# Performance work log

Measured on AMD Instinct MI355X. Metric: run time of the kernel, lower is better.

## Reference

```python
import jax, jax.numpy as jnp
import numpy as np

N_LEAVES = 4096
NF = N_LEAVES            # one-hot leaf feature dim
NN = 2 * N_LEAVES - 1    # nodes in binary backbone tree
HID = 512
T_MIN, T_MAX = 0.0, 1.0  # time_grid endpoints


def _belief_prop(node_sample, ch0, ch1, parent):
    """Postorder c/d recursion then preorder correction, as in node_embedding_site_backbone.
    Node ids are topologically ordered (children < parent), so postorder = 0..NN-1."""
    is_leaf = node_sample >= 0
    leaf_d = jax.nn.one_hot(jnp.clip(node_sample, 0), NF, dtype=jnp.float32)
    c0 = jnp.zeros((NN,), jnp.float32)
    d0 = jnp.zeros((NN, NF), jnp.float32)

    def post(carry, u):
        c, d = carry
        cc = c[ch0[u]] + c[ch1[u]]
        dd = d[ch0[u]] + d[ch1[u]]
        cu = 1.0 / (3.0 - cc)
        du = cu * dd
        cu = jnp.where(is_leaf[u], 0.0, cu)
        du = jnp.where(is_leaf[u], leaf_d[u], du)
        return (c.at[u].set(cu), d.at[u].set(du)), None

    (c, d), _ = jax.lax.scan(post, (c0, d0), jnp.arange(NN))
    root = NN - 1

    def pre(d, u):
        du = jnp.where(u == root, d[u], c[u] * d[parent[u]] + d[u])
        return d.at[u].set(du), None

    d, _ = jax.lax.scan(pre, d, jnp.arange(NN - 1, -1, -1))
    return d


def _gcn_layer(x, neigh, W, b):
    # neighbor-list GCN: mean over {self} U valid neighbors, then linear
    n = x.shape[0]
    safe = jnp.where(neigh < 0, n, neigh)  # -1 -> extra zero row
    x_ext = jnp.concatenate([x, jnp.zeros((1, x.shape[1]), x.dtype)], axis=0)
    deg = 1.0 + jnp.sum(neigh >= 0, axis=1).astype(x.dtype)
    agg = (x + x_ext[safe].sum(axis=1)) / deg[:, None]
    return agg @ W + b


def setup_inputs():
    rng = np.random.default_rng(0)
    ch0 = -np.ones(NN, np.int64)
    ch1 = -np.ones(NN, np.int64)
    parent = -np.ones(NN, np.int64)
    avail = list(range(N_LEAVES))
    for u in range(N_LEAVES, NN):  # random binary coalescent topology
        a = avail.pop(int(rng.integers(len(avail))))
        b = avail.pop(int(rng.integers(len(avail))))
        ch0[u], ch1[u] = a, b
        parent[a] = u
        parent[b] = u
        avail.append(u)
    root = NN - 1
    node_sample = np.where(np.arange(NN) < N_LEAVES, np.arange(NN), -1).astype(np.int64)
    neigh = -np.ones((NN + 1, 3), np.int64)
    for u in range(NN):
        if u == root:
            neigh[u] = [ch0[u], ch1[u], -1]
        else:
            neigh[u] = [parent[u], ch0[u], ch1[u]]
    branch_child = np.arange(NN, dtype=np.int64)
    is_root = (branch_child == root).astype(np.float32)

    key = jax.random.key(0)
    ks = jax.random.split(key, 8)
    w = lambda k, s: jax.random.normal(k, s, jnp.float32) * 0.02
    E = 4 * HID + 2
    return {
        "node_sample": jnp.asarray(node_sample),
        "ch0": jnp.asarray(ch0),
        "ch1": jnp.asarray(ch1),
        "parent": jnp.asarray(parent),
        "neigh": jnp.asarray(neigh),
        "branch_child": jnp.asarray(branch_child),
        "current_focal_leaf": 7,
        "time_value": jax.random.uniform(ks[0], (NN,), jnp.float32),
        "is_root": jnp.asarray(is_root),
        "W_gnn1": w(ks[1], (NF, HID)), "b_gnn1": jnp.zeros((HID,), jnp.float32),
        "W_gnn2": w(ks[2], (HID, HID)), "b_gnn2": jnp.zeros((HID,), jnp.float32),
        "W_h1": w(ks[3], (E, HID)), "b_h1": jnp.zeros((HID,), jnp.float32),
        "W_h2": w(ks[4], (HID, HID)), "b_h2": jnp.zeros((HID,), jnp.float32),
        "W_h3": w(ks[5], (HID, 1)), "b_h3": jnp.zeros((1,), jnp.float32),
    }


def reference(node_sample, ch0, ch1, parent, neigh, branch_child, current_focal_leaf,
              time_value, is_root, W_gnn1, b_gnn1, W_gnn2, b_gnn2,
              W_h1, b_h1, W_h2, b_h2, W_h3, b_h3):
    d = _belief_prop(node_sample, ch0, ch1, parent)                  # (NN, NF)
    focal_feat = jax.nn.one_hot(current_focal_leaf, NF, dtype=jnp.float32)
    x = jnp.concatenate([d, focal_feat[None, :]], axis=0)            # (NN+1, NF)

    h = jax.nn.relu(_gcn_layer(x, neigh, W_gnn1, b_gnn1))
    emb = _gcn_layer(h, neigh, W_gnn2, b_gnn2)                       # (NN+1, HID)

    h_focal = emb[NN]                                                # appended focal node
    h_tgt = emb[branch_child]                                        # (A, HID)
    h_f = jnp.broadcast_to(h_focal[None, :], h_tgt.shape)
    t_norm = (time_value - T_MIN) / (T_MAX - T_MIN + 1e-8)
    ef = jnp.concatenate([h_f, h_tgt, jnp.abs(h_f - h_tgt), h_f * h_tgt,
                          t_norm[:, None], is_root[:, None]], axis=-1)  # (A, 4*HID+2)

    z = jax.nn.elu(ef @ W_h1 + b_h1)
    z = jax.nn.elu(z @ W_h2 + b_h2)
    logits = (z @ W_h3 + b_h3)[:, 0]
    probs = jax.nn.softmax(logits, axis=0)
    return logits, probs, ef, emb, focal_feat
```

## Files before the change

kernel.cpp:

```cpp
#include <hip/hip_runtime.h>
#include <hip/hip_bf16.h>
#include <math.h>

#define NNODES 8191
#define ROOT   8190
#define NROWS  8192
#define FOCALR 8191
#define NLEAF  4096
#define HID    512
#define EDIM   2050

#define OUT_LOGITS 0
#define OUT_PROBS  8191
#define OUT_EF     16382
#define OUT_EMB    16807932
#define OUT_FOCAL  21002236

typedef float  f32x4 __attribute__((ext_vector_type(4)));
typedef float  f32x2 __attribute__((ext_vector_type(2)));
typedef float  floatx4 __attribute__((ext_vector_type(4)));
typedef short  short8 __attribute__((ext_vector_type(8)));
typedef unsigned short u16;
typedef unsigned short u16x8 __attribute__((ext_vector_type(8)));
typedef unsigned short u16x4 __attribute__((ext_vector_type(4)));

__device__ __forceinline__ f32x4 ldg4(const float* p) { return *(const f32x4*)p; }
__device__ __forceinline__ f32x2 ldg2(const float* p) { return *(const f32x2*)p; }
__device__ __forceinline__ void stg4(float* p, f32x4 v) { *(f32x4*)p = v; }

__device__ __forceinline__ void st_row(float* p, f32x4 v0, f32x4 v1) {
    asm volatile("global_store_dwordx4 %0, %1, off sc0 sc1\n\t"
                 "global_store_dwordx4 %0, %2, off offset:1024 sc0 sc1"
                 :: "v"(p), "v"(v0), "v"(v1) : "memory");
}
__device__ __forceinline__ void st_flag_ordered(float* p, float v) {
    asm volatile("s_waitcnt vmcnt(0)\n\tglobal_store_dword %0, %1, off sc0 sc1"
                 :: "v"(p), "v"(v) : "memory");
}
__device__ __forceinline__ void spin1(const float* pc, float& cv) {
    for (;;) {
        asm volatile("global_load_dword %0, %1, off sc0 sc1\n\ts_waitcnt vmcnt(0)"
                     : "=&v"(cv) : "v"(pc) : "memory");
        if (cv > 0.0f) break;
        __builtin_amdgcn_s_sleep(1);
    }
}
__device__ __forceinline__ void spin2(const float* pa, const float* pb,
                                      float& va, float& vb) {
    for (;;) {
        asm volatile("global_load_dword %0, %2, off sc0 sc1\n\t"
                     "global_load_dword %1, %3, off sc0 sc1\n\t"
                     "s_waitcnt vmcnt(0)"
                     : "=&v"(va), "=&v"(vb) : "v"(pa), "v"(pb) : "memory");
        if (va > 0.0f && vb > 0.0f) break;
        __builtin_amdgcn_s_sleep(1);
    }
}
__device__ __forceinline__ void spin3(const float* pa, const float* pb,
                                      const float* pc, float& va, float& vb, float& vc) {
    for (;;) {
        asm volatile("global_load_dword %0, %3, off sc0 sc1\n\t"
                     "global_load_dword %1, %4, off sc0 sc1\n\t"
                     "global_load_dword %2, %5, off sc0 sc1\n\t"
                     "s_waitcnt vmcnt(0)"
                     : "=&v"(va), "=&v"(vb), "=&v"(vc)
                     : "v"(pa), "v"(pb), "v"(pc) : "memory");
        if (va > 0.0f && vb > 0.0f && vc > 0.0f) break;
        __builtin_amdgcn_s_sleep(1);
    }
}
__device__ __forceinline__ void spin4(const float* p0, const float* p1,
                                      const float* p2, const float* p3,
                                      float& v0, float& v1, float& v2, float& v3) {
    for (;;) {
        asm volatile("global_load_dword %0, %4, off sc0 sc1\n\t"
                     "global_load_dword %1, %5, off sc0 sc1\n\t"
                     "global_load_dword %2, %6, off sc0 sc1\n\t"
                     "global_load_dword %3, %7, off sc0 sc1\n\t"
                     "s_waitcnt vmcnt(0)"
                     : "=&v"(v0), "=&v"(v1), "=&v"(v2), "=&v"(v3)
                     : "v"(p0), "v"(p1), "v"(p2), "v"(p3) : "memory");
        if (v0 > 0.0f && v1 > 0.0f && v2 > 0.0f && v3 > 0.0f) break;
        __builtin_amdgcn_s_sleep(1);
    }
}
__device__ __forceinline__ void rows1_cv(const float* p, f32x4& a0, f32x4& a1) {
    asm volatile("global_load_dwordx4 %0, %2, off sc0 sc1\n\t"
                 "global_load_dwordx4 %1, %2, off offset:1024 sc0 sc1\n\t"
                 "s_waitcnt vmcnt(0)"
                 : "=&v"(a0), "=&v"(a1) : "v"(p) : "memory");
}
__device__ __forceinline__ void rows2_cv(const float* p0, const float* p1,
                                         f32x4& a0, f32x4& a1, f32x4& b0, f32x4& b1) {
    asm volatile("global_load_dwordx4 %0, %4, off sc0 sc1\n\t"
                 "global_load_dwordx4 %1, %4, off offset:1024 sc0 sc1\n\t"
                 "global_load_dwordx4 %2, %5, off sc0 sc1\n\t"
                 "global_load_dwordx4 %3, %5, off offset:1024 sc0 sc1\n\t"
                 "s_waitcnt vmcnt(0)"
                 : "=&v"(a0), "=&v"(a1), "=&v"(b0), "=&v"(b1)
                 : "v"(p0), "v"(p1) : "memory");
}
__device__ __forceinline__ void rows3_cv(const float* p0, const float* p1,
                                         const float* p2,
                                         f32x4& a0, f32x4& a1, f32x4& b0, f32x4& b1,
                                         f32x4& c0, f32x4& c1) {
    asm volatile("global_load_dwordx4 %0, %6, off sc0 sc1\n\t"
                 "global_load_dwordx4 %1, %6, off offset:1024 sc0 sc1\n\t"
                 "global_load_dwordx4 %2, %7, off sc0 sc1\n\t"
                 "global_load_dwordx4 %3, %7, off offset:1024 sc0 sc1\n\t"
                 "global_load_dwordx4 %4, %8, off sc0 sc1\n\t"
                 "global_load_dwordx4 %5, %8, off offset:1024 sc0 sc1\n\t"
                 "s_waitcnt vmcnt(0)"
                 : "=&v"(a0), "=&v"(a1), "=&v"(b0), "=&v"(b1), "=&v"(c0), "=&v"(c1)
                 : "v"(p0), "v"(p1), "v"(p2) : "memory");
}
__device__ __forceinline__ void rows4_cv(const float* p0, const float* p1,
                                         const float* p2, const float* p3,
                                         f32x4& a0, f32x4& a1, f32x4& b0, f32x4& b1,
                                         f32x4& c0, f32x4& c1, f32x4& d0, f32x4& d1) {
    asm volatile("global_load_dwordx4 %0, %8, off sc0 sc1\n\t"
                 "global_load_dwordx4 %1, %8, off offset:1024 sc0 sc1\n\t"
                 "global_load_dwordx4 %2, %9, off sc0 sc1\n\t"
                 "global_load_dwordx4 %3, %9, off offset:1024 sc0 sc1\n\t"
                 "global_load_dwordx4 %4, %10, off sc0 sc1\n\t"
                 "global_load_dwordx4 %5, %10, off offset:1024 sc0 sc1\n\t"
                 "global_load_dwordx4 %6, %11, off sc0 sc1\n\t"
                 "global_load_dwordx4 %7, %11, off offset:1024 sc0 sc1\n\t"
                 "s_waitcnt vmcnt(0)"
                 : "=&v"(a0), "=&v"(a1), "=&v"(b0), "=&v"(b1),
                   "=&v"(c0), "=&v"(c1), "=&v"(d0), "=&v"(d1)
                 : "v"(p0), "v"(p1), "v"(p2), "v"(p3) : "memory");
}
__device__ __forceinline__ f32x4 fma4(f32x4 s, float cv, f32x4 pv) { return s + cv * pv; }

__device__ __forceinline__ u16 f2bf(float x) {
    union { float f; unsigned u; } u; u.f = x;
    unsigned r = u.u + 0x7fffu + ((u.u >> 16) & 1u);
    return (u16)(r >> 16);
}
__device__ __forceinline__ float b2f(u16 h) {
    union { unsigned u; float f; } x; x.u = ((unsigned)h) << 16; return x.f;
}

__global__ __launch_bounds__(256) void stage1_kernel(const int* __restrict__ ns,
                                                     const int* __restrict__ ch0,
                                                     const int* __restrict__ ch1,
                                                     const int* __restrict__ par,
                                                     const float* __restrict__ W1,
                                                     float* __restrict__ c,
                                                     float* __restrict__ ypost,
                                                     float* __restrict__ y,
                                                     float* __restrict__ flag2,
                                                     const float* __restrict__ W2,
                                                     const float* __restrict__ Wh2,
                                                     const float* __restrict__ Wh1,
                                                     u16* __restrict__ wte,
                                                     u16* __restrict__ wt2,
                                                     u16* __restrict__ WTz1,
                                                     const int* __restrict__ cfl,
                                                     float* __restrict__ outf,
                                                     const float* __restrict__ bh1,
                                                     float* __restrict__ bprime,
                                                     const float* __restrict__ bh3,
                                                     float* __restrict__ outlog) {
    __shared__ float tile[32][33];
    int bid = blockIdx.x, tid = threadIdx.x;

    if (bid < 256) {
        int gtid = bid * 256 + tid;
        int wave = gtid >> 6, lane = gtid & 63;
        int j0 = lane * 4;

        for (int u = NLEAF + wave; u < NNODES; u += 1024) {
            int a = ch0[u], b = ch1[u];
            int la = ns[a], lb = ns[b];
            const float *ra0, *ra1, *rb0, *rb1;
            int ga0 = -1, ga1 = -1, gb0 = -1, gb1 = -1;
            if (la >= 0) { ra0 = W1 + (long)la * HID; ra1 = ra0; }
            else {
                int x0 = ch0[a], x1 = ch1[a];
                int n0 = ns[x0], n1 = ns[x1];
                if (n0 >= 0) ra0 = W1 + (long)n0 * HID;
                else { ra0 = ypost + (long)x0 * HID; ga0 = x0; }
                if (n1 >= 0) ra1 = W1 + (long)n1 * HID;
                else { ra1 = ypost + (long)x1 * HID; ga1 = x1; }
            }
            if (lb >= 0) { rb0 = W1 + (long)lb * HID; rb1 = rb0; }
            else {
                int x0 = ch0[b], x1 = ch1[b];
                int n0 = ns[x0], n1 = ns[x1];
                if (n0 >= 0) rb0 = W1 + (long)n0 * HID;
                else { rb0 = ypost + (long)x0 * HID; gb0 = x0; }
                if (n1 >= 0) rb1 = W1 + (long)n1 * HID;
                else { rb1 = ypost + (long)x1 * HID; gb1 = x1; }
            }
            float ca0 = 0.f, ca1 = 0.f, cb0 = 0.f, cb1 = 0.f;
            if ((ga0 | ga1 | gb0 | gb1) >= 0) {
                int w0 = ga0 >= 0 ? ga0 : ga1 >= 0 ? ga1 : gb0 >= 0 ? gb0 : gb1;
                float s0, s1, s2, s3;
                spin4(c + (ga0 >= 0 ? ga0 : w0), c + (ga1 >= 0 ? ga1 : w0),
                      c + (gb0 >= 0 ? gb0 : w0), c + (gb1 >= 0 ? gb1 : w0),
                      s0, s1, s2, s3);
                if (ga0 >= 0) ca0 = s0;
                if (ga1 >= 0) ca1 = s1;
                if (gb0 >= 0) cb0 = s2;
                if (gb1 >= 0) cb1 = s3;
            }
            f32x4 qa00, qa01, qa10, qa11, qb00, qb01, qb10, qb11;
            rows4_cv(ra0 + j0, ra1 + j0, rb0 + j0, rb1 + j0,
                     qa00, qa01, qa10, qa11, qb00, qb01, qb10, qb11);
            f32x4 A0, A1, B0, B1; float cA, cB;
            if (la >= 0) { cA = 0.0f; A0 = qa00; A1 = qa01; }
            else {
                cA = 1.0f / (3.0f - (ca0 + ca1));
                A0 = (qa00 + qa10) * cA; A1 = (qa01 + qa11) * cA;
            }
            if (lb >= 0) { cB = 0.0f; B0 = qb00; B1 = qb01; }
            else {
                cB = 1.0f / (3.0f - (cb0 + cb1));
                B0 = (qb00 + qb10) * cB; B1 = (qb01 + qb11) * cB;
            }
            float cu = 1.0f / (3.0f - (cA + cB));
            st_row(ypost + (long)u * HID + j0, (A0 + B0) * cu, (A1 + B1) * cu);
            if (lane == 0) st_flag_ordered(&c[u], cu);
        }

        for (int u = ROOT - wave; u >= NLEAF; u -= 1024) {
            float* dst = y + (long)u * HID + j0;
            if (u == ROOT) {
                float cr;
                spin1(c + ROOT, cr);
                f32x4 s0, s1;
                rows1_cv(ypost + (long)ROOT * HID + j0, s0, s1);
                st_row(dst, s0, s1);
            } else {
                int p = par[u];
                if (p == ROOT) {
                    float cr, cu;
                    spin2(c + ROOT, c + u, cr, cu);
                    f32x4 s0, s1, r0, r1;
                    rows2_cv(ypost + (long)u * HID + j0, ypost + (long)ROOT * HID + j0,
                             s0, s1, r0, r1);
                    st_row(dst, fma4(s0, cu, r0), fma4(s1, cu, r1));
                } else {
                    int gp = par[p];
                    float f2, cu, cp;
                    spin3(flag2 + gp, c + u, c + p, f2, cu, cp);
                    f32x4 s0, s1, pp0, pp1, gg0, gg1;
                    rows3_cv(ypost + (long)u * HID + j0, ypost + (long)p * HID + j0,
                             y + (long)gp * HID + j0, s0, s1, pp0, pp1, gg0, gg1);
                    f32x4 yp0 = fma4(pp0, cp, gg0);
                    f32x4 yp1 = fma4(pp1, cp, gg1);
                    st_row(dst, fma4(s0, cu, yp0), fma4(s1, cu, yp1));
                }
            }
            if (lane == 0) st_flag_ordered(&flag2[u], 1.0f);
        }
        return;
    }

    if (bid < 1024) {
        int t = bid - 256;
        int bx = t & 15, by = t >> 4;
        int sec = by >> 4, kt = by & 15;
        int tx = tid & 31, ty = tid >> 5;
        int n0 = bx * 32, k0 = kt * 32;
        const float* src = (sec == 0) ? W2 : (sec == 1) ? Wh2 : (Wh1 + (long)1024 * HID);
        u16* dst = (sec == 0) ? wte : (sec == 1) ? wt2 : WTz1;
        int ld = (sec == 2) ? 1024 : 512;
        int koff = (sec == 2) ? 512 : 0;
#pragma unroll
        for (int i = 0; i < 4; i++)
            tile[ty + i * 8][tx] = src[(long)(k0 + ty + i * 8) * HID + n0 + tx];
        __syncthreads();
#pragma unroll
        for (int i = 0; i < 4; i++)
            dst[(long)(n0 + ty + i * 8) * ld + koff + k0 + tx] = f2bf(tile[tx][ty + i * 8]);
        return;
    }

    int cf = cfl[0];
    for (int i = tid; i < NLEAF; i += 256) outf[i] = (i == cf) ? 1.0f : 0.0f;
    float b3v = bh3[0];
    for (int i = tid; i < NNODES; i += 256) outlog[i] = b3v;
    for (int i = tid; i < 512; i += 256) bprime[i] = bh1[i];
}

__global__ __launch_bounds__(256) void emb_fan_kernel(const float* __restrict__ emb,
                                                      const int* __restrict__ bc,
                                                      const float* __restrict__ tv,
                                                      const float* __restrict__ isr,
                                                      float* __restrict__ ef,
                                                      const float* __restrict__ Wh1,
                                                      u16* __restrict__ WTz1,
                                                      float* __restrict__ bprime) {
    __shared__ float tB[32][33];
    __shared__ float tD[32][33];
    int bid = blockIdx.x, t = threadIdx.x;
    const float* hf = emb + (long)FOCALR * HID;

    if (bid < NNODES) {
        int u = bid;
        const float* ht = emb + (long)bc[u] * HID;
        f32x2 f = ldg2(hf + 2 * t);
        f32x2 h = ldg2(ht + 2 * t);
        float* row = ef + (long)u * EDIM;
        *(f32x2*)(row + 2 * t) = f;
        *(f32x2*)(row + 512 + 2 * t) = h;
        f32x2 d; d[0] = fabsf(f[0] - h[0]); d[1] = fabsf(f[1] - h[1]);
        *(f32x2*)(row + 1024 + 2 * t) = d;
        f32x2 p; p[0] = f[0] * h[0]; p[1] = f[1] * h[1];
        *(f32x2*)(row + 1536 + 2 * t) = p;
        if (t == 0) {
            row[2048] = tv[u];
            row[2049] = isr[u];
        }
        return;
    }
    if (bid < NNODES + 256) {
        int q = bid - NNODES;
        int tx = t & 31, ty = t >> 5;
        int n0 = (q & 15) * 32, k0 = (q >> 4) * 32;
#pragma unroll
        for (int i = 0; i < 4; i++) {
            tB[ty + i * 8][tx] = Wh1[(long)(512 + k0 + ty + i * 8) * HID + n0 + tx];
            tD[ty + i * 8][tx] = Wh1[(long)(1536 + k0 + ty + i * 8) * HID + n0 + tx];
        }
        __syncthreads();
#pragma unroll
        for (int i = 0; i < 4; i++) {
            float hfk = hf[k0 + tx];
            WTz1[(long)(n0 + ty + i * 8) * 1024 + k0 + tx] =
                f2bf(tB[tx][ty + i * 8] + hfk * tD[tx][ty + i * 8]);
        }
        return;
    }
    int kc = bid - NNODES - 256;
    float s0 = 0.0f, s1 = 0.0f;
#pragma unroll 4
    for (int k = kc * 64; k < kc * 64 + 64; k++) {
        float h = hf[k];
        s0 += h * Wh1[(long)k * HID + t];
        s1 += h * Wh1[(long)k * HID + 256 + t];
    }
    atomicAdd(bprime + t, s0);
    atomicAdd(bprime + 256 + t, s1);
}

template <int RELU, int BIAS, int OBF, int REDIR, int INBF>
__global__ __launch_bounds__(128) void gcn_agg_kernel(const float* __restrict__ xinf,
                                                      const u16* __restrict__ xinb,
                                                      const int* __restrict__ neigh,
                                                      const float* __restrict__ bias,
                                                      const int* __restrict__ ns,
                                                      const int* __restrict__ cfl,
                                                      const float* __restrict__ W1,
                                                      float* __restrict__ xoutf,
                                                      u16* __restrict__ xoutb) {
    int u = blockIdx.x;
    int t = threadIdx.x;
    int n0 = neigh[u * 3 + 0], n1 = neigh[u * 3 + 1], n2 = neigh[u * 3 + 2];
    float deg = 1.0f + (n0 >= 0) + (n1 >= 0) + (n2 >= 0);
    f32x4 s;
    if (INBF) {
        auto rdbf = [&](int v) -> f32x4 {
            u16x4 h4 = *(const u16x4*)(xinb + (long)v * HID + t * 4);
            f32x4 r; r.x = b2f(h4[0]); r.y = b2f(h4[1]); r.z = b2f(h4[2]); r.w = b2f(h4[3]);
            return r;
        };
        s = rdbf(u);
        if (n0 >= 0) s += rdbf(n0);
        if (n1 >= 0) s += rdbf(n1);
        if (n2 >= 0) s += rdbf(n2);
    } else {
        auto rowp = [&](int v) -> const float* {
            if (!REDIR) return xinf + (long)v * HID;
            if (v == FOCALR) return W1 + (long)cfl[0] * HID;
            int nv = ns[v];
            return (nv >= 0) ? (W1 + (long)nv * HID) : (xinf + (long)v * HID);
        };
        s = ldg4(rowp(u) + t * 4);
        if (n0 >= 0) s += ldg4(rowp(n0) + t * 4);
        if (n1 >= 0) s += ldg4(rowp(n1) + t * 4);
        if (n2 >= 0) s += ldg4(rowp(n2) + t * 4);
    }
    s *= (1.0f / deg);
    if (BIAS) s += ldg4(bias + t * 4);
    if (RELU) { s.x = fmaxf(s.x, 0.f); s.y = fmaxf(s.y, 0.f); s.z = fmaxf(s.z, 0.f); s.w = fmaxf(s.w, 0.f); }
    if (OBF) {
        u16x4 h; h[0] = f2bf(s.x); h[1] = f2bf(s.y); h[2] = f2bf(s.z); h[3] = f2bf(s.w);
        *(u16x4*)(xoutb + (long)u * HID + t * 4) = h;
    } else {
        stg4(xoutf + (long)u * HID + t * 4, s);
    }
}

__device__ __forceinline__ int sw_idx(int row, int kc8) {
    return (row * 8 + (kc8 ^ (row & 7))) * 8;
}

template <int ACT, int AGEN, int LOG>
__global__ __launch_bounds__(256, 3) void gemm_v5(const u16* __restrict__ Abf,
                                                  const u16* __restrict__ WT,
                                                  const float* __restrict__ bias,
                                                  const int* __restrict__ bc,
                                                  const float* __restrict__ tv,
                                                  const float* __restrict__ isr,
                                                  const float* __restrict__ Wtail,
                                                  float* __restrict__ Cf,
                                                  u16* __restrict__ Cbf,
                                                  int M, int K,
                                                  const float* __restrict__ W3,
                                                  float* __restrict__ outlog) {
    __shared__ u16 As[2][64 * 64];
    __shared__ u16 Ws[2][128 * 64];
    const int tid = threadIdx.x, lane = tid & 63;
    const int wm = (tid >> 6) >> 1, wn = (tid >> 6) & 1;
    const int bm = blockIdx.y * 64, bn = blockIdx.x * 128;
    const int kq = lane >> 4, lr = lane & 15;
    const int srow = tid >> 3, schunk = tid & 7;
    const int nk = K >> 6;
    floatx4 acc[2][4] = {};

    int btc[2];
    if (AGEN) {
#pragma unroll
        for (int i = 0; i < 2; i++) {
            int gr = bm + srow + i * 32;
            btc[i] = bc[gr < M ? gr : 0];
        }
    }

    u16x8 pf_hf, pf_a[2], pf_b[4];

    auto prefetch = [&](int kk) {
        if (AGEN) {
            int cb = (kk & 7) * 64 + schunk * 8;
            pf_hf = *(const u16x8*)(Abf + (long)FOCALR * HID + cb);
#pragma unroll
            for (int i = 0; i < 2; i++)
                pf_a[i] = *(const u16x8*)(Abf + (long)btc[i] * HID + cb);
        } else {
            long kof = (long)(kk * 64 + schunk * 8);
#pragma unroll
            for (int i = 0; i < 2; i++) {
                int gr = bm + srow + i * 32;
                if (gr < M) pf_a[i] = *(const u16x8*)(Abf + (long)gr * K + kof);
                else        pf_a[i] = (u16x8){0,0,0,0,0,0,0,0};
            }
        }
#pragma unroll
        for (int i = 0; i < 4; i++)
            pf_b[i] = *(const u16x8*)(WT + (long)(bn + srow + i * 32) * K + kk * 64 + schunk * 8);
    };

    auto commit = [&](int kk, int buf) {
        if (AGEN) {
            int sec = kk >> 3;
#pragma unroll
            for (int i = 0; i < 2; i++) {
                u16x8 v;
                if (sec == 0) v = pf_a[i];
                else {
#pragma unroll
                    for (int q = 0; q < 8; q++) v[q] = f2bf(fabsf(b2f(pf_hf[q]) - b2f(pf_a[i][q])));
                }
                if (bm + srow + i * 32 >= M) v = (u16x8){0,0,0,0,0,0,0,0};
                *(u16x8*)&As[buf][sw_idx(srow + i * 32, schunk)] = v;
            }
        } else {
#pragma unroll
            for (int i = 0; i < 2; i++)
                *(u16x8*)&As[buf][sw_idx(srow + i * 32, schunk)] = pf_a[i];
        }
#pragma unroll
        for (int i = 0; i < 4; i++)
            *(u16x8*)&Ws[buf][sw_idx(srow + i * 32, schunk)] = pf_b[i];
// ... 79 lines not shown
}

__global__ __launch_bounds__(1024) void softmax_kernel(const float* __restrict__ lg,
                                                       float* __restrict__ probs) {
    __shared__ float red[16];
    __shared__ float gmax_s, gsum_s;
    int t = threadIdx.x, wid = t >> 6, lane = t & 63;
    float m = -3.4e38f;
    for (int i = t; i < NNODES; i += 1024) m = fmaxf(m, lg[i]);
    for (int o = 32; o; o >>= 1) m = fmaxf(m, __shfl_down(m, o));
    if (lane == 0) red[wid] = m;
    __syncthreads();
    if (t == 0) {
        float g = red[0];
        for (int i = 1; i < 16; i++) g = fmaxf(g, red[i]);
        gmax_s = g;
    }
    __syncthreads();
    float gmax = gmax_s;
    float s = 0.0f;
    for (int i = t; i < NNODES; i += 1024) s += expf(lg[i] - gmax);
    for (int o = 32; o; o >>= 1) s += __shfl_down(s, o);
    if (lane == 0) red[wid] = s;
    __syncthreads();
    if (t == 0) {
        float g = 0.0f;
        for (int i = 0; i < 16; i++) g += red[i];
        gsum_s = g;
    }
    __syncthreads();
    float inv = 1.0f / gsum_s;
    for (int i = t; i < NNODES; i += 1024) probs[i] = expf(lg[i] - gmax) * inv;
}

extern "C" void kernel_launch(void* const* d_in, const int* in_sizes, int n_in,
                              void* d_out, int out_size, void* d_ws, size_t ws_size,
                              hipStream_t stream) {
    const int*   ns    = (const int*)d_in[0];
    const int*   ch0   = (const int*)d_in[1];
    const int*   ch1   = (const int*)d_in[2];
    const int*   par   = (const int*)d_in[3];
    const int*   neigh = (const int*)d_in[4];
    const int*   bc    = (const int*)d_in[5];
    const int*   cfl   = (const int*)d_in[6];
    const float* tv    = (const float*)d_in[7];
    const float* isr   = (const float*)d_in[8];
    const float* W1    = (const float*)d_in[9];
    const float* b1    = (const float*)d_in[10];
    const float* W2    = (const float*)d_in[11];
    const float* b2    = (const float*)d_in[12];
    const float* Wh1   = (const float*)d_in[13];
    const float* bh1   = (const float*)d_in[14];
    const float* Wh2   = (const float*)d_in[15];
    const float* bh2   = (const float*)d_in[16];
    const float* Wh3   = (const float*)d_in[17];
    const float* bh3   = (const float*)d_in[18];

    float* out = (float*)d_out;
    float* out_logits = out + OUT_LOGITS;
    float* out_probs  = out + OUT_PROBS;
    float* out_ef     = out + OUT_EF;
    float* out_emb    = out + OUT_EMB;
    float* out_focal  = out + OUT_FOCAL;

    const size_t MB = 1024 * 1024;
    char* ws = (char*)d_ws;
    float* c      = (float*)(ws);
    float* flag2  = (float*)(ws + 40960);
    float* buf0   = (float*)(ws + 81920);
    float* buf1   = (float*)(ws + 81920 + 16 * MB);
    float* buf2   = (float*)(ws + 81920 + 32 * MB);
    u16*   wte    = (u16*)  (ws + 81920 + 48 * MB);
    u16*   wt2    = (u16*)  (ws + 81920 + 48 * MB + 512 * 1024);
    u16*   wtz1   = (u16*)  (ws + 81920 + 49 * MB);
    float* bprime = (float*)(ws + 81920 + 50 * MB);

    float* ypost  = buf0;
    float* y      = buf1;
    u16*   a2_bf  = (u16*)buf1;
    u16*   emb_bf = (u16*)((char*)buf1 + 8 * MB);
    u16*   h_bf   = (u16*)buf2;
    u16*   z1_bf  = (u16*)buf2;

    stage1_kernel<<<dim3(1025), dim3(256), 0, stream>>>(ns, ch0, ch1, par, W1, c, ypost,
                                                        y, flag2, W2, Wh2, Wh1, wte, wt2,
                                                        wtz1, cfl, out_focal, bh1, bprime,
                                                        bh3, out_logits);
    gcn_agg_kernel<1, 1, 1, 1, 0><<<dim3(NROWS), dim3(128), 0, stream>>>(
        y, nullptr, neigh, b1, ns, cfl, W1, nullptr, h_bf);
    gcn_agg_kernel<0, 0, 1, 0, 1><<<dim3(NROWS), dim3(128), 0, stream>>>(
        nullptr, h_bf, neigh, b1, ns, cfl, W1, nullptr, a2_bf);
    gemm_v5<0, 0, 0><<<dim3(4, 128), dim3(256), 0, stream>>>(
        a2_bf, wte, b2, nullptr, nullptr, nullptr, nullptr, out_emb, emb_bf,
        NROWS, HID, nullptr, nullptr);
    emb_fan_kernel<<<dim3(NNODES + 256 + 8), dim3(256), 0, stream>>>(
        out_emb, bc, tv, isr, out_ef, Wh1, wtz1, bprime);
    gemm_v5<2, 1, 0><<<dim3(4, 128), dim3(256), 0, stream>>>(
        emb_bf, wtz1, bprime, bc, tv, isr, Wh1 + (long)2048 * HID, nullptr, z1_bf,
        NNODES, 1024, nullptr, nullptr);
    gemm_v5<2, 0, 1><<<dim3(4, 128), dim3(256), 0, stream>>>(
        z1_bf, wt2, bh2, nullptr, nullptr, nullptr, nullptr, nullptr, nullptr,
        NNODES, HID, Wh3, out_logits);
    softmax_kernel<<<dim3(1), dim3(1024), 0, stream>>>(out_logits, out_probs);
}
```

Before: 279.1 us.

## Fuse first GCN aggregation into stage1 and deepen postorder lookahead to grandchildren

Result: no change. 283.0 us (+1.4%).

```diff
diff --git a/kernel.cpp b/kernel.cpp
--- a/kernel.cpp
+++ b/kernel.cpp
@@ -45,42 +45,44 @@
         __builtin_amdgcn_s_sleep(1);
     }
 }
-__device__ __forceinline__ void spin2(const float* pa, const float* pb,
-                                      float& va, float& vb) {
+__device__ __forceinline__ void spin5(const float* p0, const float* p1, const float* p2,
+                                      const float* p3, const float* p4,
+                                      float& v0, float& v1, float& v2, float& v3,
+                                      float& v4) {
     for (;;) {
-        asm volatile("global_load_dword %0, %2, off sc0 sc1\n\t"
-                     "global_load_dword %1, %3, off sc0 sc1\n\t"
+        asm volatile("global_load_dword %0, %5, off sc0 sc1\n\t"
+                     "global_load_dword %1, %6, off sc0 sc1\n\t"
+                     "global_load_dword %2, %7, off sc0 sc1\n\t"
+                     "global_load_dword %3, %8, off sc0 sc1\n\t"
+                     "global_load_dword %4, %9, off sc0 sc1\n\t"
                      "s_waitcnt vmcnt(0)"
-                     : "=&v"(va), "=&v"(vb) : "v"(pa), "v"(pb) : "memory");
-        if (va > 0.0f && vb > 0.0f) break;
+                     : "=&v"(v0), "=&v"(v1), "=&v"(v2), "=&v"(v3), "=&v"(v4)
+                     : "v"(p0), "v"(p1), "v"(p2), "v"(p3), "v"(p4) : "memory");
+        if (v0 > 0.0f && v1 > 0.0f && v2 > 0.0f && v3 > 0.0f && v4 > 0.0f) break;
         __builtin_amdgcn_s_sleep(1);
     }
 }
-__device__ __forceinline__ void spin3(const float* pa, const float* pb,
-                                      const float* pc, float& va, float& vb, float& vc) {
+__device__ __forceinline__ void spin8(const float* p0, const float* p1, const float* p2,
+                                      const float* p3, const float* p4, const float* p5,
+                                      const float* p6, const float* p7,
+                                      float& v0, float& v1, float& v2, float& v3,
+                                      float& v4, float& v5, float& v6, float& v7) {
     for (;;) {
-        asm volatile("global_load_dword %0, %3, off sc0 sc1\n\t"
-                     "global_load_dword %1, %4, off sc0 sc1\n\t"
-                     "global_load_dword %2, %5, off sc0 sc1\n\t"
+        asm volatile("global_load_dword %0, %8, off sc0 sc1\n\t"
+                     "global_load_dword %1, %9, off sc0 sc1\n\t"
+                     "global_load_dword %2, %10, off sc0 sc1\n\t"
+                     "global_load_dword %3, %11, off sc0 sc1\n\t"
+                     "global_load_dword %4, %12, off sc0 sc1\n\t"
+                     "global_load_dword %5, %13, off sc0 sc1\n\t"
+                     "global_load_dword %6, %14, off sc0 sc1\n\t"
+                     "global_load_dword %7, %15, off sc0 sc1\n\t"
                      "s_waitcnt vmcnt(0)"
-                     : "=&v"(va), "=&v"(vb), "=&v"(vc)
-                     : "v"(pa), "v"(pb), "v"(pc) : "memory");
-        if (va > 0.0f && vb > 0.0f && vc > 0.0f) break;
-        __builtin_amdgcn_s_sleep(1);
-    }
-}
-__device__ __forceinline__ void spin4(const float* p0, const float* p1,
-                                      const float* p2, const float* p3,
-                                      float& v0, float& v1, float& v2, float& v3) {
-    for (;;) {
-        asm volatile("global_load_dword %0, %4, off sc0 sc1\n\t"
-                     "global_load_dword %1, %5, off sc0 sc1\n\t"
-                     "global_load_dword %2, %6, off sc0 sc1\n\t"
-                     "global_load_dword %3, %7, off sc0 sc1\n\t"
-                     "s_waitcnt vmcnt(0)"
-                     : "=&v"(v0), "=&v"(v1), "=&v"(v2), "=&v"(v3)
-                     : "v"(p0), "v"(p1), "v"(p2), "v"(p3) : "memory");
-        if (v0 > 0.0f && v1 > 0.0f && v2 > 0.0f && v3 > 0.0f) break;
+                     : "=&v"(v0), "=&v"(v1), "=&v"(v2), "=&v"(v3),
+                       "=&v"(v4), "=&v"(v5), "=&v"(v6), "=&v"(v7)
+                     : "v"(p0), "v"(p1), "v"(p2), "v"(p3),
+                       "v"(p4), "v"(p5), "v"(p6), "v"(p7) : "memory");
+        if (v0 > 0.0f && v1 > 0.0f && v2 > 0.0f && v3 > 0.0f &&
+            v4 > 0.0f && v5 > 0.0f && v6 > 0.0f && v7 > 0.0f) break;
         __builtin_amdgcn_s_sleep(1);
     }
 }
@@ -90,48 +92,64 @@
                  "s_waitcnt vmcnt(0)"
                  : "=&v"(a0), "=&v"(a1) : "v"(p) : "memory");
 }
-__device__ __forceinline__ void rows2_cv(const float* p0, const float* p1,
-                                         f32x4& a0, f32x4& a1, f32x4& b0, f32x4& b1) {
-    asm volatile("global_load_dwordx4 %0, %4, off sc0 sc1\n\t"
-                 "global_load_dwordx4 %1, %4, off offset:1024 sc0 sc1\n\t"
-                 "global_load_dwordx4 %2, %5, off sc0 sc1\n\t"
-                 "global_load_dwordx4 %3, %5, off offset:1024 sc0 sc1\n\t"
+__device__ __forceinline__ void rows5_cv(const float* p0, const float* p1,
+                                         const float* p2, const float* p3,
+                                         const float* p4,
+                                         f32x4& a0, f32x4& a1, f32x4& b0, f32x4& b1,
+                                         f32x4& c0, f32x4& c1, f32x4& d0, f32x4& d1,
+                                         f32x4& e0, f32x4& e1) {
+    asm volatile("global_load_dwordx4 %0, %10, off sc0 sc1\n\t"
+                 "global_load_dwordx4 %1, %10, off offset:1024 sc0 sc1\n\t"
+                 "global_load_dwordx4 %2, %11, off sc0 sc1\n\t"
+                 "global_load_dwordx4 %3, %11, off offset:1024 sc0 sc1\n\t"
+                 "global_load_dwordx4 %4, %12, off sc0 sc1\n\t"
+                 "global_load_dwordx4 %5, %12, off offset:1024 sc0 sc1\n\t"
+                 "global_load_dwordx4 %6, %13, off sc0 sc1\n\t"
+                 "global_load_dwordx4 %7, %13, off offset:1024 sc0 sc1\n\t"
+                 "global_load_dwordx4 %8, %14, off sc0 sc1\n\t"
+                 "global_load_dwordx4 %9, %14, off offset:1024 sc0 sc1\n\t"
                  "s_waitcnt vmcnt(0)"
-                 : "=&v"(a0), "=&v"(a1), "=&v"(b0), "=&v"(b1)
-                 : "v"(p0), "v"(p1) : "memory");
-}
-__device__ __forceinline__ void rows3_cv(const float* p0, const float* p1,
-                                         const float* p2,
+                 : "=&v"(a0), "=&v"(a1), "=&v"(b0), "=&v"(b1), "=&v"(c0), "=&v"(c1),
+                   "=&v"(d0), "=&v"(d1), "=&v"(e0), "=&v"(e1)
+                 : "v"(p0), "v"(p1), "v"(p2), "v"(p3), "v"(p4) : "memory");
+}
+__device__ __forceinline__ void rows8_cv(const float* p0, const float* p1,
+                                         const float* p2, const float* p3,
+                                         const float* p4, const float* p5,
+                                         const float* p6, const float* p7,
                                          f32x4& a0, f32x4& a1, f32x4& b0, f32x4& b1,
-                                         f32x4& c0, f32x4& c1) {
-    asm volatile("global_load_dwordx4 %0, %6, off sc0 sc1\n\t"
-                 "global_load_dwordx4 %1, %6, off offset:1024 sc0 sc1\n\t"
-                 "global_load_dwordx4 %2, %7, off sc0 sc1\n\t"
-                 "global_load_dwordx4 %3, %7, off offset:1024 sc0 sc1\n\t"
-                 "global_load_dwordx4 %4, %8, off sc0 sc1\n\t"
-                 "global_load_dwordx4 %5, %8, off offset:1024 sc0 sc1\n\t"
+                                         f32x4& c0, f32x4& c1, f32x4& d0, f32x4& d1,
+                                         f32x4& e0, f32x4& e1, f32x4& f0, f32x4& f1,
+                                         f32x4& g0, f32x4& g1, f32x4& h0, f32x4& h1) {
+    asm volatile("global_load_dwordx4 %0, %16, off sc0 sc1\n\t"
+                 "global_load_dwordx4 %1, %16, off offset:1024 sc0 sc1\n\t"
+                 "global_load_dwordx4 %2, %17, off sc0 sc1\n\t"
+                 "global_load_dwordx4 %3, %17, off offset:1024 sc0 sc1\n\t"
+                 "global_load_dwordx4 %4, %18, off sc0 sc1\n\t"
+                 "global_load_dwordx4 %5, %18, off offset:1024 sc0 sc1\n\t"
+                 "global_load_dwordx4 %6, %19, off sc0 sc1\n\t"
+                 "global_load_dwordx4 %7, %19, off offset:1024 sc0 sc1\n\t"
+                 "global_load_dwordx4 %8, %20, off sc0 sc1\n\t"
+                 "global_load_dwordx4 %9, %20, off offset:1024 sc0 sc1\n\t"
+                 "global_load_dwordx4 %10, %21, off sc0 sc1\n\t"
+                 "global_load_dwordx4 %11, %21, off offset:1024 sc0 sc1\n\t"
+                 "global_load_dwordx4 %12, %22, off sc0 sc1\n\t"
+                 "global_load_dwordx4 %13, %22, off offset:1024 sc0 sc1\n\t"
+                 "global_load_dwordx4 %14, %23, off sc0 sc1\n\t"
+                 "global_load_dwordx4 %15, %23, off offset:1024 sc0 sc1\n\t"
                  "s_waitcnt vmcnt(0)"
-                 : "=&v"(a0), "=&v"(a1), "=&v"(b0), "=&v"(b1), "=&v"(c0), "=&v"(c1)
-                 : "v"(p0), "v"(p1), "v"(p2) : "memory");
-}
-__device__ __forceinline__ void rows4_cv(const float* p0, const float* p1,
-                                         const float* p2, const float* p3,
-                                         f32x4& a0, f32x4& a1, f32x4& b0, f32x4& b1,
-                                         f32x4& c0, f32x4& c1, f32x4& d0, f32x4& d1) {
-    asm volatile("global_load_dwordx4 %0, %8, off sc0 sc1\n\t"
-                 "global_load_dwordx4 %1, %8, off offset:1024 sc0 sc1\n\t"
-                 "global_load_dwordx4 %2, %9, off sc0 sc1\n\t"
-                 "global_load_dwordx4 %3, %9, off offset:1024 sc0 sc1\n\t"
-                 "global_load_dwordx4 %4, %10, off sc0 sc1\n\t"
-                 "global_load_dwordx4 %5, %10, off offset:1024 sc0 sc1\n\t"
-                 "global_load_dwordx4 %6, %11, off sc0 sc1\n\t"
-                 "global_load_dwordx4 %7, %11, off offset:1024 sc0 sc1\n\t"
-                 "s_waitcnt vmcnt(0)"
-                 : "=&v"(a0), "=&v"(a1), "=&v"(b0), "=&v"(b1),
-                   "=&v"(c0), "=&v"(c1), "=&v"(d0), "=&v"(d1)
-                 : "v"(p0), "v"(p1), "v"(p2), "v"(p3) : "memory");
+                 : "=&v"(a0), "=&v"(a1), "=&v"(b0), "=&v"(b1), "=&v"(c0), "=&v"(c1),
+                   "=&v"(d0), "=&v"(d1), "=&v"(e0), "=&v"(e1), "=&v"(f0), "=&v"(f1),
+                   "=&v"(g0), "=&v"(g1), "=&v"(h0), "=&v"(h1)
+                 : "v"(p0), "v"(p1), "v"(p2), "v"(p3), "v"(p4), "v"(p5), "v"(p6),
+                   "v"(p7) : "memory");
 }
 __device__ __forceinline__ f32x4 fma4(f32x4 s, float cv, f32x4 pv) { return s + cv * pv; }
+__device__ __forceinline__ f32x4 relu4(f32x4 v) {
+    v.x = fmaxf(v.x, 0.f); v.y = fmaxf(v.y, 0.f);
+    v.z = fmaxf(v.z, 0.f); v.w = fmaxf(v.w, 0.f);
+    return v;
+}
 
 __device__ __forceinline__ u16 f2bf(float x) {
     union { float f; unsigned u; } u; u.f = x;
@@ -146,11 +164,14 @@
                                                      const int* __restrict__ ch0,
                                                      const int* __restrict__ ch1,
                                                      const int* __restrict__ par,
+                                                     const int* __restrict__ neigh,
                                                      const float* __restrict__ W1,
+                                                     const float* __restrict__ bias1,
                                                      float* __restrict__ c,
                                                      float* __restrict__ ypost,
                                                      float* __restrict__ y,
                                                      float* __restrict__ flag2,
+                                                     u16* __restrict__ h_bf,
                                                      const float* __restrict__ W2,
                                                      const float* __restrict__ Wh2,
                                                      const float* __restrict__ Wh1,
@@ -172,56 +193,85 @@
         int j0 = lane * 4;
 
         for (int u = NLEAF + wave; u < NNODES; u += 1024) {
-            int a = ch0[u], b = ch1[u];
-            int la = ns[a], lb = ns[b];
-            const float *ra0, *ra1, *rb0, *rb1;
-            int ga0 = -1, ga1 = -1, gb0 = -1, gb1 = -1;
-            if (la >= 0) { ra0 = W1 + (long)la * HID; ra1 = ra0; }
-            else {
-                int x0 = ch0[a], x1 = ch1[a];
-                int n0 = ns[x0], n1 = ns[x1];
-                if (n0 >= 0) ra0 = W1 + (long)n0 * HID;
-                else { ra0 = ypost + (long)x0 * HID; ga0 = x0; }
-                if (n1 >= 0) ra1 = W1 + (long)n1 * HID;
-                else { ra1 = ypost + (long)x1 * HID; ga1 = x1; }
+            int na = ch0[u], nb = ch1[u];
+            int la = ns[na], lb = ns[nb];
+            int s4 = -1, s5 = -1, s6 = -1, s7 = -1;
+            int l4 = 0, l5 = 0, l6 = 0, l7 = 0;
+            if (la < 0) { s4 = ch0[na]; s5 = ch1[na]; l4 = ns[s4]; l5 = ns[s5]; }
+            if (lb < 0) { s6 = ch0[nb]; s7 = ch1[nb]; l6 = ns[s6]; l7 = ns[s7]; }
+            bool e4 = (s4 >= 0) && (l4 < 0), e5 = (s5 >= 0) && (l5 < 0);
+            bool e6 = (s6 >= 0) && (l6 < 0), e7 = (s7 >= 0) && (l7 < 0);
+            int s8 = -1, s9 = -1, s10 = -1, s11 = -1, s12 = -1, s13 = -1, s14 = -1, s15 = -1;
+            int l8 = 0, l9 = 0, l10 = 0, l11 = 0, l12 = 0, l13 = 0, l14 = 0, l15 = 0;
+            if (e4) { s8  = ch0[s4]; s9  = ch1[s4]; l8  = ns[s8];  l9  = ns[s9];  }
+            if (e5) { s10 = ch0[s5]; s11 = ch1[s5]; l10 = ns[s10]; l11 = ns[s11]; }
+            if (e6) { s12 = ch0[s6]; s13 = ch1[s6]; l12 = ns[s12]; l13 = ns[s13]; }
+            if (e7) { s14 = ch0[s7]; s15 = ch1[s7]; l14 = ns[s14]; l15 = ns[s15]; }
+            bool i8  = (s8  >= 0) && (l8  < 0), i9  = (s9  >= 0) && (l9  < 0);
+            bool i10 = (s10 >= 0) && (l10 < 0), i11 = (s11 >= 0) && (l11 < 0);
+            bool i12 = (s12 >= 0) && (l12 < 0), i13 = (s13 >= 0) && (l13 < 0);
+            bool i14 = (s14 >= 0) && (l14 < 0), i15 = (s15 >= 0) && (l15 < 0);
+
+            float cz8 = 0, cz9 = 0, cz10 = 0, cz11 = 0, cz12 = 0, cz13 = 0, cz14 = 0, cz15 = 0;
+            if (i8 | i9 | i10 | i11 | i12 | i13 | i14 | i15) {
+                int w0 = i8 ? s8 : i9 ? s9 : i10 ? s10 : i11 ? s11
+                       : i12 ? s12 : i13 ? s13 : i14 ? s14 : s15;
+                float t0, t1, t2, t3, t4, t5, t6, t7;
+                spin8(c + (i8 ? s8 : w0), c + (i9 ? s9 : w0), c + (i10 ? s10 : w0),
+                      c + (i11 ? s11 : w0), c + (i12 ? s12 : w0), c + (i13 ? s13 : w0),
+                      c + (i14 ? s14 : w0), c + (i15 ? s15 : w0),
+                      t0, t1, t2, t3, t4, t5, t6, t7);
+                if (i8)  cz8  = t0; if (i9)  cz9  = t1;
+                if (i10) cz10 = t2; if (i11) cz11 = t3;
+                if (i12) cz12 = t4; if (i13) cz13 = t5;
+                if (i14) cz14 = t6; if (i15) cz15 = t7;
             }
-            if (lb >= 0) { rb0 = W1 + (long)lb * HID; rb1 = rb0; }
-            else {
-                int x0 = ch0[b], x1 = ch1[b];
-                int n0 = ns[x0], n1 = ns[x1];
-                if (n0 >= 0) rb0 = W1 + (long)n0 * HID;
-                else { rb0 = ypost + (long)x0 * HID; gb0 = x0; }
-                if (n1 >= 0) rb1 = W1 + (long)n1 * HID;
-                else { rb1 = ypost + (long)x1 * HID; gb1 = x1; }
-            }
-            float ca0 = 0.f, ca1 = 0.f, cb0 = 0.f, cb1 = 0.f;
-            if ((ga0 | ga1 | gb0 | gb1) >= 0) {
-                int w0 = ga0 >= 0 ? ga0 : ga1 >= 0 ? ga1 : gb0 >= 0 ? gb0 : gb1;
-                float s0, s1, s2, s3;
-                spin4(c + (ga0 >= 0 ? ga0 : w0), c + (ga1 >= 0 ? ga1 : w0),
-                      c + (gb0 >= 0 ? gb0 : w0), c + (gb1 >= 0 ? gb1 : w0),
-                      s0, s1, s2, s3);
-                if (ga0 >= 0) ca0 = s0;
-                if (ga1 >= 0) ca1 = s1;
-                if (gb0 >= 0) cb0 = s2;
-                if (gb1 >= 0) cb1 = s3;
-            }
-            f32x4 qa00, qa01, qa10, qa11, qb00, qb01, qb10, qb11;
-            rows4_cv(ra0 + j0, ra1 + j0, rb0 + j0, rb1 + j0,
-                     qa00, qa01, qa10, qa11, qb00, qb01, qb10, qb11);
-            f32x4 A0, A1, B0, B1; float cA, cB;
-            if (la >= 0) { cA = 0.0f; A0 = qa00; A1 = qa01; }
-            else {
-                cA = 1.0f / (3.0f - (ca0 + ca1));
-                A0 = (qa00 + qa10) * cA; A1 = (qa01 + qa11) * cA;
-            }
-            if (lb >= 0) { cB = 0.0f; B0 = qb00; B1 = qb01; }
-            else {
-                cB = 1.0f / (3.0f - (cb0 + cb1));
-                B0 = (qb00 + qb10) * cB; B1 = (qb01 + qb11) * cB;
-            }
-            float cu = 1.0f / (3.0f - (cA + cB));
-            st_row(ypost + (long)u * HID + j0, (A0 + B0) * cu, (A1 + B1) * cu);
+            const float* pr0 = (la >= 0) ? W1 + (long)la * HID + j0
+                             : !e4 ? W1 + (long)l4 * HID + j0
+                             : (l8 >= 0) ? W1 + (long)l8 * HID + j0
+                                         : ypost + (long)s8 * HID + j0;
+            const float* pr1 = e4 ? ((l9 >= 0) ? W1 + (long)l9 * HID + j0
+                                               : ypost + (long)s9 * HID + j0) : pr0;
+            const float* pr2 = (la < 0)
+                             ? (!e5 ? W1 + (long)l5 * HID + j0
+                                    : (l10 >= 0) ? W1 + (long)l10 * HID + j0
+                                                 : ypost + (long)s10 * HID + j0)
+                             : pr0;
+            const float* pr3 = e5 ? ((l11 >= 0) ? W1 + (long)l11 * HID + j0
+                                                : ypost + (long)s11 * HID + j0) : pr0;
+            const float* pr4 = (lb >= 0) ? W1 + (long)lb * HID + j0
+                             : !e6 ? W1 + (long)l6 * HID + j0
+                             : (l12 >= 0) ? W1 + (long)l12 * HID + j0
+                                          : ypost + (long)s12 * HID + j0;
+            const float* pr5 = e6 ? ((l13 >= 0) ? W1 + (long)l13 * HID + j0
+                                                : ypost + (long)s13 * HID + j0) : pr4;
+            const float* pr6 = (lb < 0)
+                             ? (!e7 ? W1 + (long)l7 * HID + j0
+                                    : (l14 >= 0) ? W1 + (long)l14 * HID + j0
+                                                 : ypost + (long)s14 * HID + j0)
+                             : pr4;
+            const float* pr7 = e7 ? ((l15 >= 0) ? W1 + (long)l15 * HID + j0
+                                                : ypost + (long)s15 * HID + j0) : pr4;
+
+            f32x4 q0a, q0b, q1a, q1b, q2a, q2b, q3a, q3b;
+            f32x4 q4a, q4b, q5a, q5b, q6a, q6b, q7a, q7b;
+            rows8_cv(pr0, pr1, pr2, pr3, pr4, pr5, pr6, pr7,
+                     q0a, q0b, q1a, q1b, q2a, q2b, q3a, q3b,
+                     q4a, q4b, q5a, q5b, q6a, q6b, q7a, q7b);
+
+            float c4v = 0, c5v = 0, c6v = 0, c7v = 0;
+            f32x4 V4a = q0a, V4b = q0b, V5a = q2a, V5b = q2b;
+            f32x4 V6a = q4a, V6b = q4b, V7a = q6a, V7b = q6b;
+            if (e4) { c4v = 1.0f / (3.0f - (cz8  + cz9));  V4a = (q0a + q1a) * c4v; V4b = (q0b + q1b) * c4v; }
+            if (e5) { c5v = 1.0f / (3.0f - (cz10 + cz11)); V5a = (q2a + q3a) * c5v; V5b = (q2b + q3b) * c5v; }
+            if (e6) { c6v = 1.0f / (3.0f - (cz12 + cz13)); V6a = (q4a + q5a) * c6v; V6b = (q4b + q5b) * c6v; }
+            if (e7) { c7v = 1.0f / (3.0f - (cz14 + cz15)); V7a = (q6a + q7a) * c7v; V7b = (q6b + q7b) * c7v; }
+            float cAv = 0, cBv = 0;
+            f32x4 Aa = q0a, Ab = q0b, Ba = q4a, Bb = q4b;
+            if (la < 0) { cAv = 1.0f / (3.0f - (c4v + c5v)); Aa = (V4a + V5a) * cAv; Ab = (V4b + V5b) * cAv; }
+            if (lb < 0) { cBv = 1.0f / (3.0f - (c6v + c7v)); Ba = (V6a + V7a) * cBv; Bb = (V6b + V7b) * cBv; }
+            float cu = 1.0f / (3.0f - (cAv + cBv));
+            st_row(ypost + (long)u * HID + j0, (Aa + Ba) * cu, (Ab + Bb) * cu);
             if (lane == 0) st_flag_ordered(&c[u], cu);
         }
 
@@ -234,27 +284,114 @@
                 rows1_cv(ypost + (long)ROOT * HID + j0, s0, s1);
                 st_row(dst, s0, s1);
             } else {
-                int p = par[u];
-                if (p == ROOT) {
-                    float cr, cu;
-                    spin2(c + ROOT, c + u, cr, cu);
-                    f32x4 s0, s1, r0, r1;
-                    rows2_cv(ypost + (long)u * HID + j0, ypost + (long)ROOT * HID + j0,
-                             s0, s1, r0, r1);
-                    st_row(dst, fma4(s0, cu, r0), fma4(s1, cu, r1));
-                } else {
-                    int gp = par[p];
-                    float f2, cu, cp;
-                    spin3(flag2 + gp, c + u, c + p, f2, cu, cp);
-                    f32x4 s0, s1, pp0, pp1, gg0, gg1;
-                    rows3_cv(ypost + (long)u * HID + j0, ypost + (long)p * HID + j0,
-                             y + (long)gp * HID + j0, s0, s1, pp0, pp1, gg0, gg1);
-                    f32x4 yp0 = fma4(pp0, cp, gg0);
-                    f32x4 yp1 = fma4(pp1, cp, gg1);
-                    st_row(dst, fma4(s0, cu, yp0), fma4(s1, cu, yp1));
-                }
+                int p1v = par[u];
+                int p2v = (p1v == ROOT) ? ROOT : par[p1v];
+                int p3v = (p2v == ROOT) ? ROOT : par[p2v];
+                int p4v = (p3v == ROOT) ? ROOT : par[p3v];
+                bool m1 = (p1v != ROOT);
+                bool m2 = m1 && (p2v != ROOT);
+                bool m3 = m2 && (p3v != ROOT);
+                bool troot = (p4v == ROOT);
+                const float* fpt = troot ? (c + ROOT) : (flag2 + p4v);
+                const float* rpt = troot ? (ypost + (long)ROOT * HID + j0)
+                                         : (y + (long)p4v * HID + j0);
+                const float* f0 = c + u;
+                const float* f1 = m1 ? c + p1v : f0;
+                const float* f2 = m2 ? c + p2v : f0;
+                const float* f3 = m3 ? c + p3v : f0;
+                float ft, cu, c1v, c2v, c3v;
+                spin5(fpt, f0, f1, f2, f3, ft, cu, c1v, c2v, c3v);
+                const float* r0 = ypost + (long)u * HID + j0;
+                const float* r1 = m1 ? ypost + (long)p1v * HID + j0 : r0;
+                const float* r2 = m2 ? ypost + (long)p2v * HID + j0 : r0;
+                const float* r3 = m3 ? ypost + (long)p3v * HID + j0 : r0;
+                f32x4 t0, t1, u0, u1, v0, v1, w0, w1, z0, z1;
+                rows5_cv(rpt, r0, r1, r2, r3, t0, t1, u0, u1, v0, v1, w0, w1, z0, z1);
+                f32x4 yv0 = t0, yv1 = t1;
+                if (m3) { yv0 = fma4(w0 * 0.0f + z0, c3v, yv0); yv1 = fma4(z1, c3v, yv1); }
+                if (m3) { }
+                if (m2) { yv0 = fma4(w0, c2v, yv0); yv1 = fma4(w1, c2v, yv1); }
+                if (m1) { yv0 = fma4(v0, c1v, yv0); yv1 = fma4(v1, c1v, yv1); }
+                yv0 = fma4(u0, cu, yv0); yv1 = fma4(u1, cu, yv1);
+                st_row(dst, yv0, yv1);
             }
             if (lane == 0) st_flag_ordered(&flag2[u], 1.0f);
+        }
+
+        int cfl0 = cfl[0];
+        for (int rr = wave; rr < NROWS; rr += 2048) {
+            int uA = rr, uB = rr + 1024;
+            int A1n = neigh[uA * 3], A2n = neigh[uA * 3 + 1], A3n = neigh[uA * 3 + 2];
+            int B1n = neigh[uB * 3], B2n = neigh[uB * 3 + 1], B3n = neigh[uB * 3 + 2];
+            float degA = 1.0f + (A1n >= 0) + (A2n >= 0) + (A3n >= 0);
+            float degB = 1.0f + (B1n >= 0) + (B2n >= 0) + (B3n >= 0);
+            bool iA0 = (uA >= NLEAF) && (uA < NNODES);
+            bool iA1 = (A1n >= NLEAF) && (A1n < NNODES);
+            bool iA2 = (A2n >= NLEAF) && (A2n < NNODES);
+            bool iA3 = (A3n >= NLEAF) && (A3n < NNODES);
+            bool iB0 = (uB >= NLEAF) && (uB < NNODES);
+            bool iB1 = (B1n >= NLEAF) && (B1n < NNODES);
+            bool iB2 = (B2n >= NLEAF) && (B2n < NNODES);
+            bool iB3 = (B3n >= NLEAF) && (B3n < NNODES);
+            f32x4 sA0 = {0, 0, 0, 0}, sA1 = {0, 0, 0, 0};
+            f32x4 sB0 = {0, 0, 0, 0}, sB1 = {0, 0, 0, 0};
+            auto lr = [&](int v) -> const float* {
+                int l = (v == FOCALR) ? cfl0 : ns[v];
+                return W1 + (long)l * HID + j0;
+            };
+            if (!iA0) { const float* p = lr(uA); sA0 += ldg4(p); sA1 += ldg4(p + 256); }
+            if (A1n >= 0 && !iA1) { const float* p = lr(A1n); sA0 += ldg4(p); sA1 += ldg4(p + 256); }
+            if (A2n >= 0 && !iA2) { const float* p = lr(A2n); sA0 += ldg4(p); sA1 += ldg4(p + 256); }
+            if (A3n >= 0 && !iA3) { const float* p = lr(A3n); sA0 += ldg4(p); sA1 += ldg4(p + 256); }
+            if (!iB0) { const float* p = lr(uB); sB0 += ldg4(p); sB1 += ldg4(p + 256); }
+            if (B1n >= 0 && !iB1) { const float* p = lr(B1n); sB0 += ldg4(p); sB1 += ldg4(p + 256); }
+            if (B2n >= 0 && !iB2) { const float* p = lr(B2n); sB0 += ldg4(p); sB1 += ldg4(p + 256); }
+            if (B3n >= 0 && !iB3) { const float* p = lr(B3n); sB0 += ldg4(p); sB1 += ldg4(p + 256); }
+            if (iA0 | iA1 | iA2 | iA3 | iB0 | iB1 | iB2 | iB3) {
+                int w0 = iA0 ? uA : iA1 ? A1n : iA2 ? A2n : iA3 ? A3n
+                       : iB0 ? uB : iB1 ? B1n : iB2 ? B2n : B3n;
+                float g0, g1, g2, g3, g4, g5, g6, g7;
+                spin8(flag2 + (iA0 ? uA : w0), flag2 + (iA1 ? A1n : w0),
+                      flag2 + (iA2 ? A2n : w0), flag2 + (iA3 ? A3n : w0),
+                      flag2 + (iB0 ? uB : w0), flag2 + (iB1 ? B1n : w0),
+                      flag2 + (iB2 ? B2n : w0), flag2 + (iB3 ? B3n : w0),
+                      g0, g1, g2, g3, g4, g5, g6, g7);
+                const float* yd = y + (long)w0 * HID + j0;
+                f32x4 x00, x01, x10, x11, x20, x21, x30, x31;
+                f32x4 x40, x41, x50, x51, x60, x61, x70, x71;
+                rows8_cv(iA0 ? y + (long)uA * HID + j0 : yd,
+                         iA1 ? y + (long)A1n * HID + j0 : yd,
+                         iA2 ? y + (long)A2n * HID + j0 : yd,
+                         iA3 ? y + (long)A3n * HID + j0 : yd,
+                         iB0 ? y + (long)uB * HID + j0 : yd,
+                         iB1 ? y + (long)B1n * HID + j0 : yd,
+                         iB2 ? y + (long)B2n * HID + j0 : yd,
+                         iB3 ? y + (long)B3n * HID + j0 : yd,
+                         x00, x01, x10, x11, x20, x21, x30, x31,
+                         x40, x41, x50, x51, x60, x61, x70, x71);
+                if (iA0) { sA0 += x00; sA1 += x01; }
+                if (iA1) { sA0 += x10; sA1 += x11; }
+                if (iA2) { sA0 += x20; sA1 += x21; }
+                if (iA3) { sA0 += x30; sA1 += x31; }
+                if (iB0) { sB0 += x40; sB1 += x41; }
+                if (iB1) { sB0 += x50; sB1 += x51; }
+                if (iB2) { sB0 += x60; sB1 += x61; }
+                if (iB3) { sB0 += x70; sB1 += x71; }
+            }
+            f32x4 bb0 = ldg4(bias1 + j0), bb1 = ldg4(bias1 + 256 + j0);
+            sA0 = relu4(sA0 * (1.0f / degA) + bb0);
+            sA1 = relu4(sA1 * (1.0f / degA) + bb1);
+            sB0 = relu4(sB0 * (1.0f / degB) + bb0);
+            sB1 = relu4(sB1 * (1.0f / degB) + bb1);
+            u16x4 hh;
+            hh[0] = f2bf(sA0.x); hh[1] = f2bf(sA0.y); hh[2] = f2bf(sA0.z); hh[3] = f2bf(sA0.w);
+            *(u16x4*)(h_bf + (long)uA * HID + j0) = hh;
+            hh[0] = f2bf(sA1.x); hh[1] = f2bf(sA1.y); hh[2] = f2bf(sA1.z); hh[3] = f2bf(sA1.w);
+            *(u16x4*)(h_bf + (long)uA * HID + 256 + j0) = hh;
+            hh[0] = f2bf(sB0.x); hh[1] = f2bf(sB0.y); hh[2] = f2bf(sB0.z); hh[3] = f2bf(sB0.w);
+            *(u16x4*)(h_bf + (long)uB * HID + j0) = hh;
+            hh[0] = f2bf(sB1.x); hh[1] = f2bf(sB1.y); hh[2] = f2bf(sB1.z); hh[3] = f2bf(sB1.w);
+            *(u16x4*)(h_bf + (long)uB * HID + 256 + j0) = hh;
         }
         return;
     }
@@ -347,52 +484,25 @@
     atomicAdd(bprime + 256 + t, s1);
 }
 
-template <int RELU, int BIAS, int OBF, int REDIR, int INBF>
-__global__ __launch_bounds__(128) void gcn_agg_kernel(const float* __restrict__ xinf,
-                                                      const u16* __restrict__ xinb,
-                                                      const int* __restrict__ neigh,
-                                                      const float* __restrict__ bias,
-                                                      const int* __restrict__ ns,
-                                                      const int* __restrict__ cfl,
-                                                      const float* __restrict__ W1,
-                                                      float* __restrict__ xoutf,
-                                                      u16* __restrict__ xoutb) {
+__global__ __launch_bounds__(128) void gcn2_kernel(const u16* __restrict__ xinb,
+                                                   const int* __restrict__ neigh,
+                                                   u16* __restrict__ xoutb) {
     int u = blockIdx.x;
     int t = threadIdx.x;
     int n0 = neigh[u * 3 + 0], n1 = neigh[u * 3 + 1], n2 = neigh[u * 3 + 2];
     float deg = 1.0f + (n0 >= 0) + (n1 >= 0) + (n2 >= 0);
-    f32x4 s;
-    if (INBF) {
-        auto rdbf = [&](int v) -> f32x4 {
-            u16x4 h4 = *(const u16x4*)(xinb + (long)v * HID + t * 4);
-            f32x4 r; r.x = b2f(h4[0]); r.y = b2f(h4[1]); r.z = b2f(h4[2]); r.w = b2f(h4[3]);
-            return r;
-        };
-        s = rdbf(u);
-        if (n0 >= 0) s += rdbf(n0);
-        if (n1 >= 0) s += rdbf(n1);
-        if (n2 >= 0) s += rdbf(n2);
-    } else {
-        auto rowp = [&](int v) -> const float* {
-            if (!REDIR) return xinf + (long)v * HID;
-            if (v == FOCALR) return W1 + (long)cfl[0] * HID;
-            int nv = ns[v];
-            return (nv >= 0) ? (W1 + (long)nv * HID) : (xinf + (long)v * HID);
-        };
-        s = ldg4(rowp(u) + t * 4);
-        if (n0 >= 0) s += ldg4(rowp(n0) + t * 4);
-        if (n1 >= 0) s += ldg4(rowp(n1) + t * 4);
-        if (n2 >= 0) s += ldg4(rowp(n2) + t * 4);
-    }
+    auto rdbf = [&](int v) -> f32x4 {
+        u16x4 h4 = *(const u16x4*)(xinb + (long)v * HID + t * 4);
+        f32x4 r; r.x = b2f(h4[0]); r.y = b2f(h4[1]); r.z = b2f(h4[2]); r.w = b2f(h4[3]);
+        return r;
+    };
+    f32x4 s = rdbf(u);
+    if (n0 >= 0) s += rdbf(n0);
+    if (n1 >= 0) s += rdbf(n1);
+    if (n2 >= 0) s += rdbf(n2);
     s *= (1.0f / deg);
-    if (BIAS) s += ldg4(bias + t * 4);
-    if (RELU) { s.x = fmaxf(s.x, 0.f); s.y = fmaxf(s.y, 0.f); s.z = fmaxf(s.z, 0.f); s.w = fmaxf(s.w, 0.f); }
-    if (OBF) {
-        u16x4 h; h[0] = f2bf(s.x); h[1] = f2bf(s.y); h[2] = f2bf(s.z); h[3] = f2bf(s.w);
-        *(u16x4*)(xoutb + (long)u * HID + t * 4) = h;
-    } else {
-        stg4(xoutf + (long)u * HID + t * 4, s);
-    }
+    u16x4 h; h[0] = f2bf(s.x); h[1] = f2bf(s.y); h[2] = f2bf(s.z); h[3] = f2bf(s.w);
+    *(u16x4*)(xoutb + (long)u * HID + t * 4) = h;
 }
 
 __device__ __forceinline__ int sw_idx(int row, int kc8) {
@@ -638,14 +748,12 @@
     u16*   h_bf   = (u16*)buf2;
     u16*   z1_bf  = (u16*)buf2;
 
-    stage1_kernel<<<dim3(1025), dim3(256), 0, stream>>>(ns, ch0, ch1, par, W1, c, ypost,
-                                                        y, flag2, W2, Wh2, Wh1, wte, wt2,
-                                                        wtz1, cfl, out_focal, bh1, bprime,
+    stage1_kernel<<<dim3(1025), dim3(256), 0, stream>>>(ns, ch0, ch1, par, neigh, W1, b1,
+                                                        c, ypost, y, flag2, h_bf,
+                                                        W2, Wh2, Wh1, wte, wt2, wtz1,
+                                                        cfl, out_focal, bh1, bprime,
                                                         bh3, out_logits);
-    gcn_agg_kernel<1, 1, 1, 1, 0><<<dim3(NROWS), dim3(128), 0, stream>>>(
-        y, nullptr, neigh, b1, ns, cfl, W1, nullptr, h_bf);
-    gcn_agg_kernel<0, 0, 1, 0, 1><<<dim3(NROWS), dim3(128), 0, stream>>>(
-        nullptr, h_bf, neigh, b1, ns, cfl, W1, nullptr, a2_bf);
+    gcn2_kernel<<<dim3(NROWS), dim3(128), 0, stream>>>(h_bf, neigh, a2_bf);
     gemm_v5<0, 0, 0><<<dim3(4, 128), dim3(256), 0, stream>>>(
         a2_bf, wte, b2, nullptr, nullptr, nullptr, nullptr, out_emb, emb_bf,
         NROWS, HID, nullptr, nullptr);
```
